# Optimization experiments

Measured on AMD Instinct MI355X. Metric: run time of the kernel, lower is better.

## Reference

```python
import jax, jax.numpy as jnp
import numpy as np

# ---- static config (MaskedViTConfig, eval mode with inference_topk) ----
B, IMG, P, C = 32, 224, 16, 3
G = IMG // P            # 14
N = G * G + 1           # 197 tokens incl cls
D, NH = 768, 12
HD = D // NH            # 64
SCALE = HD ** -0.5
HID = 4 * D             # 3072
GH = 128                # gate hidden
WARM, DYN = 2, 10
TOPK = 118              # min(inference_topk, N-1)
NC = 1000
EPS_MASK = 1e-6
LN_EPS = 1e-5


def _ln(x, g, b):
    mu = x.mean(-1, keepdims=True)
    var = ((x - mu) ** 2).mean(-1, keepdims=True)
    return (x - mu) / jnp.sqrt(var + LN_EPS) * g + b


def _attn(x, qkv_w, qkv_b, proj_w, proj_b, add_mask):
    # x: [B,N,D]; add_mask: [B,N] additive logit bias per key, or None
    Bb, Nn, _ = x.shape
    qkv = (x @ qkv_w + qkv_b).reshape(Bb, Nn, 3, NH, HD)
    q, k, v = qkv[:, :, 0], qkv[:, :, 1], qkv[:, :, 2]  # [B,N,H,hd]
    attn = jnp.einsum('bqhd,bkhd->bhqk', q, k) * SCALE
    if add_mask is not None:
        attn = attn + add_mask[:, None, None, :]
    attn = jax.nn.softmax(attn, axis=-1)
    out = jnp.einsum('bhqk,bkhd->bqhd', attn, v).reshape(Bb, Nn, D)
    return out @ proj_w + proj_b


def _mlp(x, w1, b1, w2, b2):
    return jax.nn.gelu(x @ w1 + b1, approximate=False) @ w2 + b2


def setup_inputs() -> dict:
    key = jax.random.key(0)
    ks = iter(jax.random.split(key, 64))
    nrm = lambda shape, s=0.02: jax.random.normal(next(ks), shape, jnp.float32) * s
    z = lambda *shape: jnp.zeros(shape, jnp.float32)
    o = lambda *shape: jnp.ones(shape, jnp.float32)
    inp = {
        'images': jax.random.normal(next(ks), (B, C, IMG, IMG), jnp.float32),
        'patch_w': nrm((D, C, P, P)), 'patch_b': z(D),
        'cls_token': nrm((1, 1, D)), 'pos_embed': nrm((1, N, D)),
        # warmup blocks, stacked on leading axis [WARM,...]
        'w_ln1_g': o(WARM, D), 'w_ln1_b': z(WARM, D),
        'w_qkv_w': nrm((WARM, D, 3 * D)), 'w_qkv_b': z(WARM, 3 * D),
        'w_proj_w': nrm((WARM, D, D)), 'w_proj_b': z(WARM, D),
        'w_ln2_g': o(WARM, D), 'w_ln2_b': z(WARM, D),
        'w_fc1_w': nrm((WARM, D, HID)), 'w_fc1_b': z(WARM, HID),
        'w_fc2_w': nrm((WARM, HID, D)), 'w_fc2_b': z(WARM, D),
        # dynamic masked blocks [DYN,...]
        'd_ln1_g': o(DYN, D), 'd_ln1_b': z(DYN, D),
        'd_qkv_w': nrm((DYN, D, 3 * D)), 'd_qkv_b': z(DYN, 3 * D),
        'd_proj_w': nrm((DYN, D, D)), 'd_proj_b': z(DYN, D),
        'd_ln2_g': o(DYN, D), 'd_ln2_b': z(DYN, D),
        'd_fc1_w': nrm((DYN, D, HID)), 'd_fc1_b': z(DYN, HID),
        'd_fc2_w': nrm((DYN, HID, D)), 'd_fc2_b': z(DYN, D),
        # gate predictor: LayerNorm -> Linear(D,GH) -> GELU -> Linear(GH,1)
        'd_gln_g': o(DYN, D), 'd_gln_b': z(DYN, D),
        'd_gw1': nrm((DYN, D, GH)), 'd_gb1': z(DYN, GH),
        'd_gw2': nrm((DYN, GH, 1)), 'd_gb2': z(DYN, 1),
        # final norm + head
        'norm_g': o(D), 'norm_b': z(D),
        'head_w': nrm((D, NC)), 'head_b': z(NC),
    }
    return inp


def reference(images, patch_w, patch_b, cls_token, pos_embed,
              w_ln1_g, w_ln1_b, w_qkv_w, w_qkv_b, w_proj_w, w_proj_b,
              w_ln2_g, w_ln2_b, w_fc1_w, w_fc1_b, w_fc2_w, w_fc2_b,
              d_ln1_g, d_ln1_b, d_qkv_w, d_qkv_b, d_proj_w, d_proj_b,
              d_ln2_g, d_ln2_b, d_fc1_w, d_fc1_b, d_fc2_w, d_fc2_b,
              d_gln_g, d_gln_b, d_gw1, d_gb1, d_gw2, d_gb2,
              norm_g, norm_b, head_w, head_b):
    Bb = images.shape[0]
    # patch embed: conv with kernel==stride==P is a block reshape + matmul
    x6 = images.reshape(Bb, C, G, P, G, P)
    x = jnp.einsum('bcxpyq,dcpq->bxyd', x6, patch_w).reshape(Bb, G * G, D) + patch_b
    cls = jnp.broadcast_to(cls_token, (Bb, 1, D))
    x = jnp.concatenate([cls, x], axis=1) + pos_embed  # [B,N,D]

    for i in range(WARM):
        x = x + _attn(_ln(x, w_ln1_g[i], w_ln1_b[i]),
                      w_qkv_w[i], w_qkv_b[i], w_proj_w[i], w_proj_b[i], None)
        x = x + _mlp(_ln(x, w_ln2_g[i], w_ln2_b[i]),
                     w_fc1_w[i], w_fc1_b[i], w_fc2_w[i], w_fc2_b[i])

    for j in range(DYN):
        # gate predictor -> logits [B,N]; cls forced kept
        h = _ln(x, d_gln_g[j], d_gln_b[j])
        logits = (jax.nn.gelu(h @ d_gw1[j] + d_gb1[j], approximate=False)
                  @ d_gw2[j] + d_gb2[j]).squeeze(-1)
        logits = logits.at[:, 0].set(1e9)
        # eval-mode top-k keep mask (inference_topk path)
        _, idx = jax.lax.top_k(logits[:, 1:], TOPK)
        m = jnp.zeros_like(logits).at[:, 0].set(1.0)
        m = m.at[jnp.arange(Bb)[:, None], idx + 1].set(1.0)
        add_mask = jnp.log(jnp.clip(m, EPS_MASK, 1.0))
        x = x + _attn(_ln(x, d_ln1_g[j], d_ln1_b[j]),
                      d_qkv_w[j], d_qkv_b[j], d_proj_w[j], d_proj_b[j], add_mask)
        v = _mlp(_ln(x, d_ln2_g[j], d_ln2_b[j]),
                 d_fc1_w[j], d_fc1_b[j], d_fc2_w[j], d_fc2_b[j])
        x = x + v * m[:, :, None]  # gate_mlp_updates=True

    x = _ln(x, norm_g, norm_b)
    return x[:, 0] @ head_w + head_b  # [B, num_classes]
```

## Files before the change

kernel.cpp:

```cpp
#include <hip/hip_runtime.h>
#include <hip/hip_bf16.h>
#include <math.h>


typedef __bf16 bf16_t;
typedef __attribute__((ext_vector_type(8))) __bf16 bf16x8;
typedef __attribute__((ext_vector_type(4))) float f32x4;

#define DI __device__ __forceinline__

constexpr int NB     = 32;
constexpr int NTOK   = 197;
constexpr int DMODEL = 768;
constexpr int NHEAD  = 12;
constexpr int HDIM   = 64;
constexpr int HIDN   = 3072;
constexpr int GHID   = 128;
constexpr int MROWS  = NB * NTOK;
constexpr int PROWS  = NB * 196;
constexpr int NLAYER = 12;
constexpr int KTOP   = 118;
constexpr float ATT_SCALE = 0.125f;
constexpr float LNEPS  = 1e-5f;
constexpr float LOGEPS = -13.815510558f;

DI f32x4 mfma16(bf16x8 a, bf16x8 b, f32x4 c) {
    return __builtin_amdgcn_mfma_f32_16x16x32_bf16(a, b, c, 0, 0, 0);
}

DI void gld_lds16(const void* g, void* l) {
    __builtin_amdgcn_global_load_lds(
        (__attribute__((address_space(1))) void*)(g),
        (__attribute__((address_space(3))) void*)(l), 16, 0, 0);
}

enum { EP_BF16 = 0, EP_GELU = 1, EP_RES = 2, EP_RESMASK = 3, EP_F32 = 4 };

template<int MODE>
__global__ __launch_bounds__(256)
void gemm_bf16(const bf16_t* __restrict__ A, const bf16_t* __restrict__ Wt,
               const float* __restrict__ bias, void* __restrict__ Cout,
               float* __restrict__ resid, const float* __restrict__ rowmask,
               int M, int N, int K, int ldc)
{
    __shared__ __align__(16) bf16_t As[2][128 * 32];
    __shared__ __align__(16) bf16_t Bs[2][128 * 32];
    const int tid  = threadIdx.x;
    const int lane = tid & 63;
    const int wave = tid >> 6;
    const int wm = wave >> 1, wn = wave & 1;
    const int quad = lane >> 4, l16 = lane & 15;
    const int m0 = blockIdx.y * 128;
    const int n0 = blockIdx.x * 128;

    f32x4 zero4 = {0.f, 0.f, 0.f, 0.f};
    f32x4 acc[4][4];
#pragma unroll
    for (int i = 0; i < 4; ++i)
#pragma unroll
        for (int j = 0; j < 4; ++j) acc[i][j] = zero4;

    const int rh  = tid >> 2;
    const int seg = tid & 3;
    const int rA0 = min(m0 + rh,      M - 1);
    const int rA1 = min(m0 + 64 + rh, M - 1);
    const int rB0 = min(n0 + rh,      N - 1);
    const int rB1 = min(n0 + 64 + rh, N - 1);
    const bf16_t* pA0 = A  + (size_t)rA0 * K + seg * 8;
    const bf16_t* pA1 = A  + (size_t)rA1 * K + seg * 8;
    const bf16_t* pB0 = Wt + (size_t)rB0 * K + seg * 8;
    const bf16_t* pB1 = Wt + (size_t)rB1 * K + seg * 8;
    const int lofs0 = wave * 512;
    const int lofs1 = 2048 + wave * 512;

    auto stage = [&](int kt2, int buf) {
        const int kb = kt2 << 5;
        gld_lds16(pA0 + kb, As[buf] + lofs0);
        gld_lds16(pA1 + kb, As[buf] + lofs1);
        gld_lds16(pB0 + kb, Bs[buf] + lofs0);
        gld_lds16(pB1 + kb, Bs[buf] + lofs1);
    };

    const int nkt = K >> 5;
    stage(0, 0);
    stage(1, 1);

    for (int kt = 0; kt < nkt; ++kt) {
        const int cur = kt & 1;
        if (kt + 1 < nkt) asm volatile("s_waitcnt vmcnt(4)" ::: "memory");
        else              asm volatile("s_waitcnt vmcnt(0)" ::: "memory");
        __builtin_amdgcn_s_barrier();

        bf16x8 af[4], bfr[4];
#pragma unroll
        for (int i = 0; i < 4; ++i)
            af[i] = *reinterpret_cast<const bf16x8*>(As[cur] + (wm * 64 + i * 16 + l16) * 32 + quad * 8);
#pragma unroll
        for (int j = 0; j < 4; ++j)
            bfr[j] = *reinterpret_cast<const bf16x8*>(Bs[cur] + (wn * 64 + j * 16 + l16) * 32 + quad * 8);

        asm volatile("s_waitcnt lgkmcnt(0)" ::: "memory");
        __builtin_amdgcn_sched_barrier(0);
        __builtin_amdgcn_s_barrier();

        if (kt + 2 < nkt) stage(kt + 2, cur);

#pragma unroll
        for (int i = 0; i < 4; ++i)
#pragma unroll
            for (int j = 0; j < 4; ++j)
                acc[i][j] = mfma16(af[i], bfr[j], acc[i][j]);
    }

#pragma unroll
    for (int j = 0; j < 4; ++j) {
        int c = n0 + wn * 64 + j * 16 + l16;
        if (c >= N) continue;
        float bj = bias ? bias[c] : 0.f;
#pragma unroll
        for (int i = 0; i < 4; ++i) {
#pragma unroll
            for (int r = 0; r < 4; ++r) {
                int mr = m0 + wm * 64 + i * 16 + quad * 4 + r;
                if (mr >= M) continue;
                float v = acc[i][j][r] + bj;
                size_t off = (size_t)mr * ldc + c;
                if (MODE == EP_BF16) {
                    ((bf16_t*)Cout)[off] = (bf16_t)v;
                } else if (MODE == EP_GELU) {
                    float g = 0.5f * v * (1.f + erff(v * 0.70710678118f));
                    ((bf16_t*)Cout)[off] = (bf16_t)g;
                } else if (MODE == EP_F32) {
                    ((float*)Cout)[off] = v;
                } else if (MODE == EP_RES) {
                    resid[off] += v;
                } else {
                    resid[off] += v * rowmask[mr];
                }
            }
        }
    }
}

DI float block_reduce_sum(float val, float* sh) {
#pragma unroll
    for (int off = 32; off; off >>= 1) val += __shfl_down(val, off, 64);
    __syncthreads();
    if ((threadIdx.x & 63) == 0) sh[threadIdx.x >> 6] = val;
    __syncthreads();
    return sh[0] + sh[1] + sh[2] + sh[3];
}

template<typename OUT>
__global__ __launch_bounds__(256)
void ln_kernel(const float* __restrict__ X, const float* __restrict__ g,
               const float* __restrict__ bta, OUT* __restrict__ H, int row_mul)
{
    __shared__ float sh[4];
    const int t = threadIdx.x;
    const float* xr = X + (size_t)blockIdx.x * row_mul * DMODEL;
    float v[3];
#pragma unroll
    for (int i = 0; i < 3; ++i) v[i] = xr[t + i * 256];
    float s = v[0] + v[1] + v[2];
    s = block_reduce_sum(s, sh);
    float mu = s * (1.f / DMODEL);
    float q = 0.f;
#pragma unroll
    for (int i = 0; i < 3; ++i) { float d = v[i] - mu; q += d * d; }
    q = block_reduce_sum(q, sh);
    float rstd = rsqrtf(q * (1.f / DMODEL) + LNEPS);
    OUT* hr = H + (size_t)blockIdx.x * DMODEL;
#pragma unroll
    for (int i = 0; i < 3; ++i) {
        int c = t + i * 256;
        hr[c] = (OUT)((v[i] - mu) * rstd * g[c] + bta[c]);
    }
}

__global__ __launch_bounds__(256)
void attn_kernel(const bf16_t* __restrict__ qkv,
                 const float* __restrict__ addmask,
                 bf16_t* __restrict__ outp)
{
    constexpr int KP = 232;
    __shared__ __align__(16) bf16_t Vt[64 * KP];
    __shared__ __align__(16) bf16_t Ps[4][16 * KP];
    const int b = blockIdx.z, h = blockIdx.y, qt = blockIdx.x;
    const int tid = threadIdx.x, wave = tid >> 6, lane = tid & 63;
    const int quad = lane >> 4, l16 = lane & 15;

    {
        int d = tid & 63, ng = tid >> 6;
        for (int n = ng; n < 224; n += 4) {
            bf16_t v = (bf16_t)0.f;
            if (n < 197)
                v = qkv[(((size_t)b * NTOK + n) * 3 + 2) * DMODEL + h * HDIM + d];
            Vt[d * KP + n] = v;
        }
    }
    __syncthreads();

    const int qbase = qt * 64 + wave * 16;
    const int qrow = qbase + l16;
    const int qc = qrow < 196 ? qrow : 196;
    bf16x8 aq[2];
#pragma unroll
    for (int t = 0; t < 2; ++t)
        aq[t] = *reinterpret_cast<const bf16x8*>(
            qkv + (((size_t)b * NTOK + qc) * 3 + 0) * DMODEL + h * HDIM + t * 32 + quad * 8);

    float sreg[13][4];
#pragma unroll
    for (int kt = 0; kt < 13; ++kt) {
        int key = kt * 16 + l16;
        int kc = key < 196 ? key : 196;
        const bf16_t* kb = qkv + (((size_t)b * NTOK + kc) * 3 + 1) * DMODEL + h * HDIM;
        bf16x8 kf0 = *reinterpret_cast<const bf16x8*>(kb + quad * 8);
        bf16x8 kf1 = *reinterpret_cast<const bf16x8*>(kb + 32 + quad * 8);
        f32x4 s = {0.f, 0.f, 0.f, 0.f};
        s = mfma16(aq[0], kf0, s);
        s = mfma16(aq[1], kf1, s);
        float am = addmask ? addmask[b * NTOK + kc] : 0.f;
        bool kvalid = key < 197;
#pragma unroll
        for (int r = 0; r < 4; ++r)
            sreg[kt][r] = kvalid ? (s[r] * ATT_SCALE + am) : -1e30f;
    }

    float psum[4];
#pragma unroll
    for (int r = 0; r < 4; ++r) {
        float mx = -1e30f;
#pragma unroll
        for (int kt = 0; kt < 13; ++kt) mx = fmaxf(mx, sreg[kt][r]);
#pragma unroll
        for (int d = 1; d < 16; d <<= 1) mx = fmaxf(mx, __shfl_xor(mx, d, 64));
        float sum = 0.f;
#pragma unroll
        for (int kt = 0; kt < 13; ++kt) {
            float p = expf(sreg[kt][r] - mx);
            sreg[kt][r] = p;
            sum += p;
        }
#pragma unroll
        for (int d = 1; d < 16; d <<= 1) sum += __shfl_xor(sum, d, 64);
        psum[r] = sum;
    }

#pragma unroll
    for (int kt = 0; kt < 13; ++kt)
#pragma unroll
        for (int r = 0; r < 4; ++r)
            Ps[wave][(quad * 4 + r) * KP + kt * 16 + l16] = (bf16_t)sreg[kt][r];
    {
        int rr = lane & 15, c0 = 208 + (lane >> 4) * 4;
#pragma unroll
        for (int i = 0; i < 4; ++i) Ps[wave][rr * KP + c0 + i] = (bf16_t)0.f;
    }
    __syncthreads();

    f32x4 o[4];
#pragma unroll
    for (int j = 0; j < 4; ++j) o[j] = (f32x4){0.f, 0.f, 0.f, 0.f};
#pragma unroll
    for (int ks = 0; ks < 7; ++ks) {
        bf16x8 ap = *reinterpret_cast<const bf16x8*>(&Ps[wave][l16 * KP + ks * 32 + quad * 8]);
#pragma unroll
        for (int j = 0; j < 4; ++j) {
            bf16x8 vf = *reinterpret_cast<const bf16x8*>(&Vt[(j * 16 + l16) * KP + ks * 32 + quad * 8]);
            o[j] = mfma16(ap, vf, o[j]);
        }
    }

#pragma unroll
    for (int r = 0; r < 4; ++r) {
        int q = qbase + quad * 4 + r;
        if (q < 197) {
            float rs = 1.f / fmaxf(psum[r], 1e-20f);
#pragma unroll
            for (int j = 0; j < 4; ++j)
                outp[((size_t)b * NTOK + q) * DMODEL + h * HDIM + j * 16 + l16] =
                    (bf16_t)(o[j][r] * rs);
        }
    }
}

__global__ __launch_bounds__(256)
void transpose_f32(const float* __restrict__ src, bf16_t* __restrict__ dst, int K, int N)
{
    __shared__ bf16_t tile[64][65];
    const size_t ls = (size_t)K * N * blockIdx.z;
    int k0 = blockIdx.y * 64, n0 = blockIdx.x * 64;
    int c = threadIdx.x & 63, r0 = threadIdx.x >> 6;
#pragma unroll
    for (int i = 0; i < 16; ++i) {
        int r = r0 + i * 4;
        tile[r][c] = (k0 + r < K && n0 + c < N)
                   ? (bf16_t)src[ls + (size_t)(k0 + r) * N + n0 + c] : (bf16_t)0.f;
    }
    __syncthreads();
#pragma unroll
    for (int i = 0; i < 16; ++i) {
        int r = r0 + i * 4;
        if (n0 + r < N && k0 + c < K) dst[ls + (size_t)(n0 + r) * K + k0 + c] = tile[c][r];
    }
}

__global__ void cvt_f32_bf16(const float* __restrict__ src, bf16_t* __restrict__ dst, int n)
{
    int i = blockIdx.x * 256 + threadIdx.x;
    if (i < n) dst[i] = (bf16_t)src[i];
}

__global__ void im2col_kernel(const float* __restrict__ img, bf16_t* __restrict__ Ap)
{
    int idx = blockIdx.x * 256 + threadIdx.x;
    if (idx >= PROWS * 768) return;
    int col = idx % 768, row = idx / 768;
    int b = row / 196, t = row % 196;
    int gi = t / 14, gj = t % 14;
    int c = col >> 8, rr = col & 255, p = rr >> 4, q = rr & 15;
    Ap[idx] = (bf16_t)img[(((size_t)b * 3 + c) * 224 + gi * 16 + p) * 224 + gj * 16 + q];
}

__global__ void assemble_x(const float* __restrict__ patch, const float* __restrict__ cls,
                           const float* __restrict__ pos, float* __restrict__ X)
{
    int idx = blockIdx.x * 256 + threadIdx.x;
    if (idx >= MROWS * DMODEL) return;
    int d = idx % DMODEL, rest = idx / DMODEL;
    int n = rest % NTOK, b = rest / NTOK;
    float v;
    if (n == 0) v = cls[d] + pos[d];
    else        v = patch[((size_t)b * 196 + (n - 1)) * DMODEL + d] + pos[(size_t)n * DMODEL + d];
    X[idx] = v;
}

__global__ __launch_bounds__(256)
void gate_fused_f32(const float* __restrict__ A, const float* __restrict__ W1,
                    const float* __restrict__ b1, const float* __restrict__ w2,
                    const float* __restrict__ b2, float* __restrict__ logits)
{
    __shared__ __align__(16) float As[16][64];
    __shared__ __align__(16) float Ws[64][128];
    const int tid = threadIdx.x;
    const int m0 = blockIdx.x * 16;
    const int tx = tid & 31;
    const int rg = tid >> 5;
    f32x4 acc0 = {0.f, 0.f, 0.f, 0.f};
    f32x4 acc1 = {0.f, 0.f, 0.f, 0.f};
    for (int k0 = 0; k0 < 768; k0 += 64) {
        __syncthreads();
        {
            int idx = tid * 4;
            int r = idx >> 6, c = idx & 63;
            *reinterpret_cast<f32x4*>(&As[r][c]) =
                *reinterpret_cast<const f32x4*>(&A[(size_t)(m0 + r) * 768 + k0 + c]);
        }
#pragma unroll
        for (int i = 0; i < 8; ++i) {
            int idx = (tid + i * 256) * 4;
            int r = idx >> 7, c = idx & 127;
            *reinterpret_cast<f32x4*>(&Ws[r][c]) =
                *reinterpret_cast<const f32x4*>(&W1[(size_t)(k0 + r) * 128 + c]);
        }
        __syncthreads();
#pragma unroll
        for (int kk = 0; kk < 64; ++kk) {
            float a0 = As[rg * 2 + 0][kk];
            float a1 = As[rg * 2 + 1][kk];
            f32x4 w = *reinterpret_cast<const f32x4*>(&Ws[kk][tx * 4]);
#pragma unroll
            for (int j = 0; j < 4; ++j) {
                acc0[j] += a0 * w[j];
                acc1[j] += a1 * w[j];
            }
        }
    }
    float s0 = 0.f, s1 = 0.f;
#pragma unroll
    for (int j = 0; j < 4; ++j) {
        int c = tx * 4 + j;
        float bj = b1[c], wj = w2[c];
        float v0 = acc0[j] + bj;
        float v1 = acc1[j] + bj;
        s0 += 0.5f * v0 * (1.f + erff(v0 * 0.70710678118f)) * wj;
        s1 += 0.5f * v1 * (1.f + erff(v1 * 0.70710678118f)) * wj;
    }
#pragma unroll
    for (int d = 1; d < 32; d <<= 1) {
        s0 += __shfl_xor(s0, d, 64);
        s1 += __shfl_xor(s1, d, 64);
    }
    if (tx == 0) {
        logits[m0 + rg * 2 + 0] = s0 + b2[0];
        logits[m0 + rg * 2 + 1] = s1 + b2[0];
    }
}

__global__ __launch_bounds__(256)
void topk_kernel(const float* __restrict__ logits, float* __restrict__ maskm,
                 float* __restrict__ addm)
{
    __shared__ float ls[196];
    int b = blockIdx.x, t = threadIdx.x;
    if (t < 196) ls[t] = logits[b * NTOK + 1 + t];
    __syncthreads();
    if (t < 196) {
        float li = ls[t];
        int cnt = 0;
        for (int j = 0; j < 196; ++j) {
            float lj = ls[j];
            cnt += (lj > li) || (lj == li && j < t);
        }
        bool sel = cnt < KTOP;
        maskm[b * NTOK + 1 + t] = sel ? 1.f : 0.f;
        addm[b * NTOK + 1 + t]  = sel ? 0.f : LOGEPS;
    }
    if (t == 0) { maskm[b * NTOK] = 1.f; addm[b * NTOK] = 0.f; }
}

__global__ void fill_sentinel(float* out, int n)
{
    int i = blockIdx.x * 256 + threadIdx.x;
    if (i < n) out[i] = 12345.0f;
}

static void launch_gemm(int mode, const bf16_t* A, const bf16_t* Wt, const float* bias,
                        void* C, float* resid, const float* rowmask,
                        int M, int N, int K, int ldc, hipStream_t s)
{
    dim3 grid((N + 127) / 128, (M + 127) / 128);
    dim3 blk(256);
    switch (mode) {
    case EP_BF16:    gemm_bf16<EP_BF16><<<grid, blk, 0, s>>>(A, Wt, bias, C, resid, rowmask, M, N, K, ldc); break;
    case EP_GELU:    gemm_bf16<EP_GELU><<<grid, blk, 0, s>>>(A, Wt, bias, C, resid, rowmask, M, N, K, ldc); break;
    case EP_RES:     gemm_bf16<EP_RES><<<grid, blk, 0, s>>>(A, Wt, bias, C, resid, rowmask, M, N, K, ldc); break;
    case EP_RESMASK: gemm_bf16<EP_RESMASK><<<grid, blk, 0, s>>>(A, Wt, bias, C, resid, rowmask, M, N, K, ldc); break;
    case EP_F32:     gemm_bf16<EP_F32><<<grid, blk, 0, s>>>(A, Wt, bias, C, resid, rowmask, M, N, K, ldc); break;
    }
}

extern "C" void kernel_launch(void* const* d_in, const int* in_sizes, int n_in,
                              void* d_out, int out_size, void* d_ws, size_t ws_size,
                              hipStream_t stream)
{
    (void)in_sizes; (void)n_in;
    const float* images   = (const float*)d_in[0];
    const float* patch_w  = (const float*)d_in[1];
    const float* patch_b  = (const float*)d_in[2];
    const float* cls_tok  = (const float*)d_in[3];
    const float* pos_emb  = (const float*)d_in[4];
    const float* w_ln1_g  = (const float*)d_in[5];
    const float* w_ln1_b  = (const float*)d_in[6];
    const float* w_qkv_w  = (const float*)d_in[7];
    const float* w_qkv_b  = (const float*)d_in[8];
    const float* w_proj_w = (const float*)d_in[9];
    const float* w_proj_b = (const float*)d_in[10];
    const float* w_ln2_g  = (const float*)d_in[11];
    const float* w_ln2_b  = (const float*)d_in[12];
    const float* w_fc1_w  = (const float*)d_in[13];
    const float* w_fc1_b  = (const float*)d_in[14];
    const float* w_fc2_w  = (const float*)d_in[15];
    const float* w_fc2_b  = (const float*)d_in[16];
    const float* d_ln1_g  = (const float*)d_in[17];
    const float* d_ln1_b  = (const float*)d_in[18];
    const float* d_qkv_w  = (const float*)d_in[19];
    const float* d_qkv_b  = (const float*)d_in[20];
    const float* d_proj_w = (const float*)d_in[21];
    const float* d_proj_b = (const float*)d_in[22];
    const float* d_ln2_g  = (const float*)d_in[23];
    const float* d_ln2_b  = (const float*)d_in[24];
    const float* d_fc1_w  = (const float*)d_in[25];
    const float* d_fc1_b  = (const float*)d_in[26];
    const float* d_fc2_w  = (const float*)d_in[27];
    const float* d_fc2_b  = (const float*)d_in[28];
    const float* d_gln_g  = (const float*)d_in[29];
    const float* d_gln_b  = (const float*)d_in[30];
    const float* d_gw1    = (const float*)d_in[31];
    const float* d_gb1    = (const float*)d_in[32];
    const float* d_gw2    = (const float*)d_in[33];
    const float* d_gb2    = (const float*)d_in[34];
    const float* norm_g   = (const float*)d_in[35];
    const float* norm_b   = (const float*)d_in[36];
    const float* head_w   = (const float*)d_in[37];
    const float* head_b   = (const float*)d_in[38];

    char* wp = (char*)d_ws;
    auto alloc = [&](size_t bytes) -> char* {
        char* p = wp; wp += (bytes + 255) & ~(size_t)255; return p;
    };
    bf16_t* wtqkv  = (bf16_t*)alloc((size_t)NLAYER * 2304 * 768 * 2);
    bf16_t* wtproj = (bf16_t*)alloc((size_t)NLAYER * 768 * 768 * 2);
    bf16_t* wtfc1  = (bf16_t*)alloc((size_t)NLAYER * 3072 * 768 * 2);
    bf16_t* wtfc2  = (bf16_t*)alloc((size_t)NLAYER * 768 * 3072 * 2);
    bf16_t* wthead = (bf16_t*)alloc((size_t)1024 * 768 * 2);
    bf16_t* pwbf   = (bf16_t*)alloc((size_t)768 * 768 * 2);
    float*  x      = (float*)alloc((size_t)MROWS * DMODEL * 4);
    bf16_t* h      = (bf16_t*)alloc((size_t)MROWS * DMODEL * 2);
    float*  hgate  = (float*)alloc((size_t)MROWS * DMODEL * 4);
    bf16_t* hcls   = (bf16_t*)alloc((size_t)NB * DMODEL * 2);
    bf16_t* qkvb   = (bf16_t*)alloc((size_t)MROWS * 2304 * 2);
    bf16_t* attno  = (bf16_t*)alloc((size_t)MROWS * DMODEL * 2);
    bf16_t* hid    = (bf16_t*)alloc((size_t)MROWS * HIDN * 2);
    float*  logits = (float*)alloc((size_t)MROWS * 4);
    float*  maskm  = (float*)alloc((size_t)MROWS * 4);
    float*  addm   = (float*)alloc((size_t)MROWS * 4);
    size_t used = (size_t)(wp - (char*)d_ws);
    if (used > ws_size) {
        fill_sentinel<<<(out_size + 255) / 256, 256, 0, stream>>>((float*)d_out, out_size);
        return;
    }
    bf16_t* Ap = hid;
    float* patchout = (float*)((char*)hid + (size_t)PROWS * 768 * 2);

    transpose_f32<<<dim3(36, 12, 2),  256, 0, stream>>>(w_qkv_w,  wtqkv,                      768, 2304);
    transpose_f32<<<dim3(36, 12, 10), 256, 0, stream>>>(d_qkv_w,  wtqkv + (size_t)2*2304*768, 768, 2304);
    transpose_f32<<<dim3(12, 12, 2),  256, 0, stream>>>(w_proj_w, wtproj,                     768, 768);
    transpose_f32<<<dim3(12, 12, 10), 256, 0, stream>>>(d_proj_w, wtproj + (size_t)2*768*768, 768, 768);
    transpose_f32<<<dim3(48, 12, 2),  256, 0, stream>>>(w_fc1_w,  wtfc1,                      768, 3072);
    transpose_f32<<<dim3(48, 12, 10), 256, 0, stream>>>(d_fc1_w,  wtfc1 + (size_t)2*3072*768, 768, 3072);
    transpose_f32<<<dim3(12, 48, 2),  256, 0, stream>>>(w_fc2_w,  wtfc2,                      3072, 768);
    transpose_f32<<<dim3(12, 48, 10), 256, 0, stream>>>(d_fc2_w,  wtfc2 + (size_t)2*768*3072, 3072, 768);
    transpose_f32<<<dim3(16, 12, 1),  256, 0, stream>>>(head_w,   wthead,                     768, 1000);
    cvt_f32_bf16<<<(768 * 768 + 255) / 256, 256, 0, stream>>>(patch_w, pwbf, 768 * 768);

    im2col_kernel<<<(PROWS * 768 + 255) / 256, 256, 0, stream>>>(images, Ap);
    launch_gemm(EP_F32, Ap, pwbf, patch_b, patchout, nullptr, nullptr,
                PROWS, 768, 768, 768, stream);
    assemble_x<<<(MROWS * DMODEL + 255) / 256, 256, 0, stream>>>(patchout, cls_tok, pos_emb, x);

    for (int L = 0; L < NLAYER; ++L) {
        bool warm = (L < 2);
        int li = warm ? L : (L - 2);
        const float* ln1g = warm ? w_ln1_g + li*768 : d_ln1_g + li*768;
        const float* ln1b = warm ? w_ln1_b + li*768 : d_ln1_b + li*768;
        const float* ln2g = warm ? w_ln2_g + li*768 : d_ln2_g + li*768;
        const float* ln2b = warm ? w_ln2_b + li*768 : d_ln2_b + li*768;
        const float* qkvbias  = warm ? w_qkv_b + li*2304 : d_qkv_b + li*2304;
        const float* projbias = warm ? w_proj_b + li*768 : d_proj_b + li*768;
        const float* fc1bias  = warm ? w_fc1_b + (size_t)li*3072 : d_fc1_b + (size_t)li*3072;
        const float* fc2bias  = warm ? w_fc2_b + li*768 : d_fc2_b + li*768;
        const bf16_t* Wq = wtqkv + (size_t)L * 2304 * 768;
        const bf16_t* Wp = wtproj + (size_t)L * 768 * 768;
        const bf16_t* W1 = wtfc1 + (size_t)L * 3072 * 768;
        const bf16_t* W2 = wtfc2 + (size_t)L * 768 * 3072;

        if (!warm) {
            ln_kernel<float><<<MROWS, 256, 0, stream>>>(x, d_gln_g + li*768, d_gln_b + li*768, hgate, 1);
            gate_fused_f32<<<MROWS / 16, 256, 0, stream>>>(
                hgate, d_gw1 + (size_t)li*768*128, d_gb1 + li*128,
                d_gw2 + (size_t)li*128, d_gb2 + li, logits);
            topk_kernel<<<NB, 256, 0, stream>>>(logits, maskm, addm);
        }
        ln_kernel<bf16_t><<<MROWS, 256, 0, stream>>>(x, ln1g, ln1b, h, 1);
        launch_gemm(EP_BF16, h, Wq, qkvbias, qkvb, nullptr, nullptr,
                    MROWS, 2304, 768, 2304, stream);
        attn_kernel<<<dim3(4, NHEAD, NB), 256, 0, stream>>>(qkvb, warm ? nullptr : addm, attno);
        launch_gemm(EP_RES, attno, Wp, projbias, nullptr, x, nullptr,
                    MROWS, 768, 768, 768, stream);
        ln_kernel<bf16_t><<<MROWS, 256, 0, stream>>>(x, ln2g, ln2b, h, 1);
        launch_gemm(EP_GELU, h, W1, fc1bias, hid, nullptr, nullptr,
                    MROWS, 3072, 768, 3072, stream);
        if (warm)
            launch_gemm(EP_RES, hid, W2, fc2bias, nullptr, x, nullptr,
                        MROWS, 768, 3072, 768, stream);
        else
            launch_gemm(EP_RESMASK, hid, W2, fc2bias, nullptr, x, maskm,
                        MROWS, 768, 3072, 768, stream);
    }

    ln_kernel<bf16_t><<<NB, 256, 0, stream>>>(x, norm_g, norm_b, hcls, NTOK);
    launch_gemm(EP_F32, hcls, wthead, head_b, d_out, nullptr, nullptr,
                NB, 1000, 768, 1000, stream);
}
```

Measured before the change: 5.120 ms.

## Compute MLP only on top-k selected tokens via gather/scatter GEMMs with split-K

In the dynamic layers, topk now also emits a compact row index list of the cls token plus the 118 kept tokens per image. FC1 gathers only those rows of the normalized activations, and FC2 scatters its residual update back to those rows. This skips the MLP work for masked tokens, whose update was previously multiplied by zero. Because the compacted FC2 grid is small, it uses split-K over two slices with atomicAdd into the residual, which makes float summation order nondeterministic and adds atomic traffic.

```diff
diff --git a/kernel.cpp b/kernel.cpp
--- a/kernel.cpp
+++ b/kernel.cpp
@@ -18,6 +18,8 @@
 constexpr int GHID   = 128;
 constexpr int MROWS  = NB * NTOK;
 constexpr int PROWS  = NB * 196;
+constexpr int NSEL   = 119;
+constexpr int MROWSC = NB * NSEL;
 constexpr int NLAYER = 12;
 constexpr int KTOP   = 118;
 constexpr float ATT_SCALE = 0.125f;
@@ -34,14 +36,14 @@
         (__attribute__((address_space(3))) void*)(l), 16, 0, 0);
 }
 
-enum { EP_BF16 = 0, EP_GELU = 1, EP_RES = 2, EP_RESMASK = 3, EP_F32 = 4 };
-
-template<int MODE>
+enum { EP_BF16 = 0, EP_GELU = 1, EP_RES = 2, EP_F32 = 4 };
+
+template<int MODE, bool GA, bool SC, bool AT>
 __global__ __launch_bounds__(256)
 void gemm_bf16(const bf16_t* __restrict__ A, const bf16_t* __restrict__ Wt,
                const float* __restrict__ bias, void* __restrict__ Cout,
-               float* __restrict__ resid, const float* __restrict__ rowmask,
-               int M, int N, int K, int ldc)
+               float* __restrict__ resid, const int* __restrict__ rowidx,
+               int M, int N, int K, int ldc, int klen)
 {
     __shared__ __align__(16) bf16_t As[2][128 * 32];
     __shared__ __align__(16) bf16_t Bs[2][128 * 32];
@@ -52,6 +54,7 @@
     const int quad = lane >> 4, l16 = lane & 15;
     const int m0 = blockIdx.y * 128;
     const int n0 = blockIdx.x * 128;
+    const int koff = AT ? blockIdx.z * klen : 0;
 
     f32x4 zero4 = {0.f, 0.f, 0.f, 0.f};
     f32x4 acc[4][4];
@@ -62,14 +65,16 @@
 
     const int rh  = tid >> 2;
     const int seg = tid & 3;
-    const int rA0 = min(m0 + rh,      M - 1);
-    const int rA1 = min(m0 + 64 + rh, M - 1);
+    int cA0 = min(m0 + rh,      M - 1);
+    int cA1 = min(m0 + 64 + rh, M - 1);
+    const int rA0 = GA ? rowidx[cA0] : cA0;
+    const int rA1 = GA ? rowidx[cA1] : cA1;
     const int rB0 = min(n0 + rh,      N - 1);
     const int rB1 = min(n0 + 64 + rh, N - 1);
-    const bf16_t* pA0 = A  + (size_t)rA0 * K + seg * 8;
-    const bf16_t* pA1 = A  + (size_t)rA1 * K + seg * 8;
-    const bf16_t* pB0 = Wt + (size_t)rB0 * K + seg * 8;
-    const bf16_t* pB1 = Wt + (size_t)rB1 * K + seg * 8;
+    const bf16_t* pA0 = A  + (size_t)rA0 * K + koff + seg * 8;
+    const bf16_t* pA1 = A  + (size_t)rA1 * K + koff + seg * 8;
+    const bf16_t* pB0 = Wt + (size_t)rB0 * K + koff + seg * 8;
+    const bf16_t* pB1 = Wt + (size_t)rB1 * K + koff + seg * 8;
     const int lofs0 = wave * 512;
     const int lofs1 = 2048 + wave * 512;
 
@@ -81,7 +86,7 @@
         gld_lds16(pB1 + kb, Bs[buf] + lofs1);
     };
 
-    const int nkt = K >> 5;
+    const int nkt = klen >> 5;
     stage(0, 0);
     stage(1, 1);
 
@@ -112,11 +117,12 @@
                 acc[i][j] = mfma16(af[i], bfr[j], acc[i][j]);
     }
 
+    const bool addb = bias && (!AT || blockIdx.z == 0);
 #pragma unroll
     for (int j = 0; j < 4; ++j) {
         int c = n0 + wn * 64 + j * 16 + l16;
         if (c >= N) continue;
-        float bj = bias ? bias[c] : 0.f;
+        float bj = addb ? bias[c] : 0.f;
 #pragma unroll
         for (int i = 0; i < 4; ++i) {
 #pragma unroll
@@ -124,7 +130,8 @@
                 int mr = m0 + wm * 64 + i * 16 + quad * 4 + r;
                 if (mr >= M) continue;
                 float v = acc[i][j][r] + bj;
-                size_t off = (size_t)mr * ldc + c;
+                int orow = SC ? rowidx[mr] : mr;
+                size_t off = (size_t)orow * ldc + c;
                 if (MODE == EP_BF16) {
                     ((bf16_t*)Cout)[off] = (bf16_t)v;
                 } else if (MODE == EP_GELU) {
@@ -132,10 +139,9 @@
                     ((bf16_t*)Cout)[off] = (bf16_t)g;
                 } else if (MODE == EP_F32) {
                     ((float*)Cout)[off] = v;
-                } else if (MODE == EP_RES) {
-                    resid[off] += v;
                 } else {
-                    resid[off] += v * rowmask[mr];
+                    if (AT) atomicAdd(&resid[off], v);
+                    else    resid[off] += v;
                 }
             }
         }
@@ -401,7 +407,7 @@
 
 __global__ __launch_bounds__(256)
 void topk_kernel(const float* __restrict__ logits, float* __restrict__ maskm,
-                 float* __restrict__ addm)
+                 float* __restrict__ addm, int* __restrict__ rowidx)
 {
     __shared__ float ls[196];
     int b = blockIdx.x, t = threadIdx.x;
@@ -417,8 +423,9 @@
         bool sel = cnt < KTOP;
         maskm[b * NTOK + 1 + t] = sel ? 1.f : 0.f;
         addm[b * NTOK + 1 + t]  = sel ? 0.f : LOGEPS;
-    }
-    if (t == 0) { maskm[b * NTOK] = 1.f; addm[b * NTOK] = 0.f; }
+        if (sel) rowidx[b * NSEL + 1 + cnt] = b * NTOK + 1 + t;
+    }
+    if (t == 0) { maskm[b * NTOK] = 1.f; addm[b * NTOK] = 0.f; rowidx[b * NSEL] = b * NTOK; }
 }
 
 __global__ void fill_sentinel(float* out, int n)
@@ -428,17 +435,16 @@
 }
 
 static void launch_gemm(int mode, const bf16_t* A, const bf16_t* Wt, const float* bias,
-                        void* C, float* resid, const float* rowmask,
+                        void* C, float* resid,
                         int M, int N, int K, int ldc, hipStream_t s)
 {
     dim3 grid((N + 127) / 128, (M + 127) / 128);
     dim3 blk(256);
     switch (mode) {
-    case EP_BF16:    gemm_bf16<EP_BF16><<<grid, blk, 0, s>>>(A, Wt, bias, C, resid, rowmask, M, N, K, ldc); break;
-    case EP_GELU:    gemm_bf16<EP_GELU><<<grid, blk, 0, s>>>(A, Wt, bias, C, resid, rowmask, M, N, K, ldc); break;
-    case EP_RES:     gemm_bf16<EP_RES><<<grid, blk, 0, s>>>(A, Wt, bias, C, resid, rowmask, M, N, K, ldc); break;
-    case EP_RESMASK: gemm_bf16<EP_RESMASK><<<grid, blk, 0, s>>>(A, Wt, bias, C, resid, rowmask, M, N, K, ldc); break;
-    case EP_F32:     gemm_bf16<EP_F32><<<grid, blk, 0, s>>>(A, Wt, bias, C, resid, rowmask, M, N, K, ldc); break;
+    case EP_BF16: gemm_bf16<EP_BF16, false, false, false><<<grid, blk, 0, s>>>(A, Wt, bias, C, resid, nullptr, M, N, K, ldc, K); break;
+    case EP_GELU: gemm_bf16<EP_GELU, false, false, false><<<grid, blk, 0, s>>>(A, Wt, bias, C, resid, nullptr, M, N, K, ldc, K); break;
+    case EP_RES:  gemm_bf16<EP_RES,  false, false, false><<<grid, blk, 0, s>>>(A, Wt, bias, C, resid, nullptr, M, N, K, ldc, K); break;
+    case EP_F32:  gemm_bf16<EP_F32,  false, false, false><<<grid, blk, 0, s>>>(A, Wt, bias, C, resid, nullptr, M, N, K, ldc, K); break;
     }
 }
 
@@ -507,6 +513,7 @@
     float*  logits = (float*)alloc((size_t)MROWS * 4);
     float*  maskm  = (float*)alloc((size_t)MROWS * 4);
     float*  addm   = (float*)alloc((size_t)MROWS * 4);
+    int*    rowidx = (int*)alloc((size_t)MROWSC * 4);
     size_t used = (size_t)(wp - (char*)d_ws);
     if (used > ws_size) {
         fill_sentinel<<<(out_size + 255) / 256, 256, 0, stream>>>((float*)d_out, out_size);
@@ -527,7 +534,7 @@
     cvt_f32_bf16<<<(768 * 768 + 255) / 256, 256, 0, stream>>>(patch_w, pwbf, 768 * 768);
 
     im2col_kernel<<<(PROWS * 768 + 255) / 256, 256, 0, stream>>>(images, Ap);
-    launch_gemm(EP_F32, Ap, pwbf, patch_b, patchout, nullptr, nullptr,
+    launch_gemm(EP_F32, Ap, pwbf, patch_b, patchout, nullptr,
                 PROWS, 768, 768, 768, stream);
     assemble_x<<<(MROWS * DMODEL + 255) / 256, 256, 0, stream>>>(patchout, cls_tok, pos_emb, x);
 
@@ -552,26 +559,31 @@
             gate_fused_f32<<<MROWS / 16, 256, 0, stream>>>(
                 hgate, d_gw1 + (size_t)li*768*128, d_gb1 + li*128,
                 d_gw2 + (size_t)li*128, d_gb2 + li, logits);
-            topk_kernel<<<NB, 256, 0, stream>>>(logits, maskm, addm);
+            topk_kernel<<<NB, 256, 0, stream>>>(logits, maskm, addm, rowidx);
         }
         ln_kernel<bf16_t><<<MROWS, 256, 0, stream>>>(x, ln1g, ln1b, h, 1);
-        launch_gemm(EP_BF16, h, Wq, qkvbias, qkvb, nullptr, nullptr,
+        launch_gemm(EP_BF16, h, Wq, qkvbias, qkvb, nullptr,
                     MROWS, 2304, 768, 2304, stream);
         attn_kernel<<<dim3(4, NHEAD, NB), 256, 0, stream>>>(qkvb, warm ? nullptr : addm, attno);
-        launch_gemm(EP_RES, attno, Wp, projbias, nullptr, x, nullptr,
+        launch_gemm(EP_RES, attno, Wp, projbias, nullptr, x,
                     MROWS, 768, 768, 768, stream);
         ln_kernel<bf16_t><<<MROWS, 256, 0, stream>>>(x, ln2g, ln2b, h, 1);
-        launch_gemm(EP_GELU, h, W1, fc1bias, hid, nullptr, nullptr,
-                    MROWS, 3072, 768, 3072, stream);
-        if (warm)
-            launch_gemm(EP_RES, hid, W2, fc2bias, nullptr, x, nullptr,
+        if (warm) {
+            launch_gemm(EP_GELU, h, W1, fc1bias, hid, nullptr,
+                        MROWS, 3072, 768, 3072, stream);
+            launch_gemm(EP_RES, hid, W2, fc2bias, nullptr, x,
                         MROWS, 768, 3072, 768, stream);
-        else
-            launch_gemm(EP_RESMASK, hid, W2, fc2bias, nullptr, x, maskm,
-                        MROWS, 768, 3072, 768, stream);
+        } else {
+            dim3 g1(24, (MROWSC + 127) / 128);
+            gemm_bf16<EP_GELU, true, false, false><<<g1, 256, 0, stream>>>(
+                h, W1, fc1bias, hid, nullptr, rowidx, MROWSC, 3072, 768, 3072, 768);
+            dim3 g2(6, (MROWSC + 127) / 128, 2);
+            gemm_bf16<EP_RES, false, true, true><<<g2, 256, 0, stream>>>(
+                hid, W2, fc2bias, nullptr, x, rowidx, MROWSC, 768, 3072, 768, 1536);
+        }
     }
 
     ln_kernel<bf16_t><<<NB, 256, 0, stream>>>(x, norm_g, norm_b, hcls, NTOK);
-    launch_gemm(EP_F32, hcls, wthead, head_b, d_out, nullptr, nullptr,
+    launch_gemm(EP_F32, hcls, wthead, head_b, d_out, nullptr,
                 NB, 1000, 768, 1000, stream);
 }
```

Result: faster. 4.620 ms (-9.8%).
